# Performance work log

Hardware: AMD Instinct MI355X
Metric: run time of the kernel (lower is better)

Reference implementation:

```python
import jax, jax.numpy as jnp
import numpy as np

B, C, H, W = 4, 256, 64, 64
EPS = 1e-6


def setup_inputs() -> dict:
    key = jax.random.key(0)
    ks = jax.random.split(key, 6)
    x = jax.random.normal(ks[0], (B, C, H, W), jnp.float32)
    gn_w = jnp.ones((1, C, 1, 1), jnp.float32)
    gn_b = jnp.zeros((1, C, 1, 1), jnp.float32)
    s = 1.0 / np.sqrt(C)
    w0 = jax.random.normal(ks[1], (C, C), jnp.float32) * s
    w1 = jax.random.normal(ks[2], (C, C), jnp.float32) * s
    w2 = jax.random.normal(ks[3], (C, C), jnp.float32) * s
    w3 = jax.random.normal(ks[4], (C, C), jnp.float32) * s
    b0 = jnp.zeros((C,), jnp.float32)
    b1 = jnp.zeros((C,), jnp.float32)
    b2 = jnp.zeros((C,), jnp.float32)
    b3 = jnp.zeros((C,), jnp.float32)
    return {"x": x, "gn_w": gn_w, "gn_b": gn_b,
            "w0": w0, "b0": b0, "w1": w1, "b1": b1,
            "w2": w2, "b2": b2, "w3": w3, "b3": b3}


def _nin(t, Wm, bv):
    # 1x1 conv as channel matmul: (B,C,H,W) x (C,D) -> (B,D,H,W)
    return jnp.einsum('bchw,cd->bdhw', t, Wm) + bv[None, :, None, None]


def reference(x, gn_w, gn_b, w0, b0, w1, b1, w2, b2, w3, b3):
    Bb, Cc, Hh, Ww = x.shape
    G = min(Cc // 4, 32)  # GroupLayerNorm2d groups
    # per-pixel group norm: normalize over channels within each group only
    xg = x.reshape(Bb, G, Cc // G, Hh, Ww)
    mean = xg.mean(axis=2, keepdims=True)
    var = xg.var(axis=2, keepdims=True)
    hn = ((xg - mean) / jnp.sqrt(var + EPS)).reshape(Bb, Cc, Hh, Ww)
    hn = hn * gn_w + gn_b
    q = _nin(hn, w0, b0)
    k = _nin(hn, w1, b1)
    v = _nin(hn, w2, b2)
    # full (B,H,W,H,W) scores; mask is causal along W only (key col j > query col w)
    scores = jnp.einsum('bchw,bcij->bhwij', q, k) * (float(Cc) ** -0.5)
    causal = jnp.triu(jnp.ones((Ww, Ww), bool), k=1)  # (W_query, W_key)
    scores = jnp.where(causal[None, None, :, None, :], -jnp.inf, scores)
    attn = jax.nn.softmax(scores.reshape(Bb, Hh, Ww, Hh * Ww), axis=-1)
    attn = attn.reshape(Bb, Hh, Ww, Hh, Ww)
    h = jnp.einsum('bhwij,bcij->bchw', attn, v)
    return x + _nin(h, w3, b3)  # skip_rescale=False
```

## Files before the change

### kernel.cpp

```cpp
#include <hip/hip_runtime.h>
#include <math.h>

#define LOG2E 1.4426950408889634f

typedef __attribute__((ext_vector_type(8))) __bf16 bf16x8_t;
typedef __attribute__((ext_vector_type(8))) short short8_t;
typedef __attribute__((ext_vector_type(4))) short short4_t;
typedef __attribute__((ext_vector_type(4))) float f32x4;

static __device__ __forceinline__ short f2bf(float f){
    unsigned u = __builtin_bit_cast(unsigned, f);
    unsigned r = (u + 0x7fffu + ((u >> 16) & 1u)) >> 16;
    return (short)r;
}
static __device__ __forceinline__ float bf2f(short s){
    return __builtin_bit_cast(float, (unsigned)((unsigned short)s) << 16);
}

static __device__ __forceinline__ f32x4 mfma16(short8_t a, short8_t b, f32x4 c){
    return __builtin_amdgcn_mfma_f32_16x16x32_bf16(
        __builtin_bit_cast(bf16x8_t, a), __builtin_bit_cast(bf16x8_t, b), c, 0, 0, 0);
}

static __device__ __forceinline__ float swz16(float v){
    return __builtin_bit_cast(float,
        __builtin_amdgcn_ds_swizzle(__builtin_bit_cast(int, v), 0x401F));
}
static __device__ __forceinline__ float bperm32(int addr, float v){
    return __builtin_bit_cast(float,
        __builtin_amdgcn_ds_bpermute(addr, __builtin_bit_cast(int, v)));
}

__global__ __launch_bounds__(256) void prep_w(const float* __restrict__ w0,
    const float* __restrict__ w1, const float* __restrict__ w2,
    const float* __restrict__ w3, short* __restrict__ wT)
{
    __shared__ float T[64 * 65];
    const int mat = blockIdx.x >> 4, tile = blockIdx.x & 15;
    const int c0 = (tile >> 2) * 64, d0 = (tile & 3) * 64;
    const float* src = mat == 0 ? w0 : mat == 1 ? w1 : mat == 2 ? w2 : w3;
    const int t = threadIdx.x;
    #pragma unroll
    for (int i = 0; i < 4; i++){
        int r = (t >> 4) + i * 16, c4 = (t & 15) * 4;
        f32x4 v = *(const f32x4*)(src + (size_t)(c0 + r) * 256 + d0 + c4);
        #pragma unroll
        for (int j = 0; j < 4; j++) T[r * 65 + c4 + j] = v[j];
    }
    __syncthreads();
    int drow = t >> 2, cb = (t & 3) * 16;
    short tmp[16];
    #pragma unroll
    for (int j = 0; j < 16; j++) tmp[j] = f2bf(T[(cb + j) * 65 + drow]);
    short* dst = wT + (size_t)mat * 65536 + (size_t)(d0 + drow) * 256 + c0 + cb;
    *(short8_t*)dst = *(short8_t*)tmp;
    *(short8_t*)(dst + 8) = *(short8_t*)(tmp + 8);
}

__global__ __launch_bounds__(256) void gn_kernel(const float* __restrict__ x,
    const float* __restrict__ gnw, const float* __restrict__ gnb,
    short* __restrict__ hn)
{
    int flat = blockIdx.x * 256 + threadIdx.x;
    int n = flat & 4095, g = (flat >> 12) & 31, b = flat >> 17;
    const float* xp = x + (size_t)(b * 256 + g * 8) * 4096 + n;
    float v[8], s = 0.f, s2 = 0.f;
    #pragma unroll
    for (int k = 0; k < 8; k++){ float t = xp[(size_t)k * 4096]; v[k] = t; s += t; s2 += t * t; }
    float mean = s * 0.125f;
    float var  = s2 * 0.125f - mean * mean;
    float inv  = rsqrtf(var + 1e-6f);
    int h = n >> 6, w = n & 63, m = w * 64 + h;
    short o[8];
    #pragma unroll
    for (int k = 0; k < 8; k++)
        o[k] = f2bf((v[k] - mean) * inv * gnw[g * 8 + k] + gnb[g * 8 + k]);
    *(short8_t*)(hn + (size_t)(b * 4096 + m) * 256 + g * 8) = *(short8_t*)o;
}

__global__ __launch_bounds__(256) void qkv_gemm(const short* __restrict__ hn,
    const short* __restrict__ wT, const float* __restrict__ bq,
    const float* __restrict__ bk, const float* __restrict__ bv,
    short* __restrict__ Q, short* __restrict__ Kf, short* __restrict__ Vf)
{
    __shared__ short As[64 * 72];
    __shared__ short Bs[64 * 72];
    __shared__ float CT[64 * 65];

    const int tid = threadIdx.x;
    const int m0 = blockIdx.x * 64;
    const int by = blockIdx.y;
    const int mat = by >> 2;
    const int d0 = (by & 3) * 64;
    const short* w = wT + mat * 65536;
    const float* bias = mat == 0 ? bq : mat == 1 ? bk : bv;

    const int wv = tid >> 6, lane = tid & 63;
    const int wrow = (wv >> 1) * 32, wcol = (wv & 1) * 32;
    const int lrow = lane & 15, lq = lane >> 4;

    f32x4 acc[2][2] = {};

    for (int k0 = 0; k0 < 256; k0 += 64){
        __syncthreads();
        #pragma unroll
        for (int i = 0; i < 2; i++){
            int idx = tid + i * 256, r = idx >> 3, c = (idx & 7) * 8;
            *(short8_t*)&As[r * 72 + c] = *(const short8_t*)(hn + (size_t)(m0 + r) * 256 + k0 + c);
            *(short8_t*)&Bs[r * 72 + c] = *(const short8_t*)(w  + (size_t)(d0 + r) * 256 + k0 + c);
        }
        __syncthreads();
        #pragma unroll
        for (int kk = 0; kk < 2; kk++){
            int off = kk * 32 + lq * 8;
            short8_t a0  = *(short8_t*)&As[(wrow + lrow) * 72 + off];
            short8_t a1  = *(short8_t*)&As[(wrow + 16 + lrow) * 72 + off];
            short8_t b0v = *(short8_t*)&Bs[(wcol + lrow) * 72 + off];
            short8_t b1v = *(short8_t*)&Bs[(wcol + 16 + lrow) * 72 + off];
            acc[0][0] = mfma16(a0, b0v, acc[0][0]);
            acc[0][1] = mfma16(a0, b1v, acc[0][1]);
            acc[1][0] = mfma16(a1, b0v, acc[1][0]);
            acc[1][1] = mfma16(a1, b1v, acc[1][1]);
        }
    }

    const int b = m0 >> 12, kb64 = (m0 & 4095) >> 6;

    if (mat == 0){
        #pragma unroll
        for (int i = 0; i < 2; i++)
          #pragma unroll
          for (int j = 0; j < 2; j++)
            #pragma unroll
            for (int r = 0; r < 4; r++){
                int row = wrow + i * 16 + lq * 4 + r;
                int col = wcol + j * 16 + lrow;
                Q[(size_t)(m0 + row) * 256 + d0 + col] = f2bf((acc[i][j][r] + bias[d0 + col]) * 0.0625f);
            }
    } else if (mat == 1){
        #pragma unroll
        for (int i = 0; i < 2; i++)
          #pragma unroll
          for (int j = 0; j < 2; j++)
            #pragma unroll
            for (int r = 0; r < 4; r++){
                int row = wrow + i * 16 + lq * 4 + r;
                int col = wcol + j * 16 + lrow;
                CT[row * 65 + col] = acc[i][j][r] + bias[d0 + col];
            }
        __syncthreads();
        int key = tid >> 2, c16 = (tid & 3) * 16;
        int kc = key >> 4, l15 = key & 15;
        #pragma unroll
        for (int half = 0; half < 2; half++){
            int ch0 = c16 + half * 8;
            int ks = (d0 + ch0) >> 5, lqf = (ch0 & 31) >> 3;
            short tmp[8];
            #pragma unroll
            for (int j = 0; j < 8; j++) tmp[j] = f2bf(CT[key * 65 + ch0 + j]);
            size_t base = ((((size_t)(b * 64 + kb64)) * 4 + kc) * 8 + ks) * 512 + (lqf * 16 + l15) * 8;
            *(short8_t*)(Kf + base) = *(short8_t*)tmp;
        }
    } else {
        #pragma unroll
        for (int i = 0; i < 2; i++)
          #pragma unroll
          for (int j = 0; j < 2; j++)
            #pragma unroll
            for (int r = 0; r < 4; r++){
                int row = wrow + i * 16 + lq * 4 + r;
                int col = wcol + j * 16 + lrow;
                CT[col * 65 + row] = acc[i][j][r] + bias[d0 + col];
            }
        __syncthreads();
        const int kbd = kb64 >> 1, parity = kb64 & 1;
        const int cht_l = tid >> 6, lane_s = tid & 63;
        const int l15s = lane_s & 15, lg4s = lane_s >> 4;
        const int cht = (d0 >> 4) + cht_l;
        #pragma unroll
        for (int kc = 0; kc < 4; kc++){
            short tmp[4];
            #pragma unroll
            for (int j = 0; j < 4; j++)
                tmp[j] = f2bf(CT[(cht_l * 16 + l15s) * 65 + kc * 16 + lg4s * 4 + j]);
            size_t base = (size_t)b * 1048576 + (size_t)kbd * 32768 + kc * 8192
                        + cht * 512 + lane_s * 8 + parity * 4;
            *(short4_t*)(Vf + base) = *(short4_t*)tmp;
        }
    }
}

__global__ __launch_bounds__(256, 2) void attn_kernel(const short* __restrict__ Q,
    const short* __restrict__ Kf, const short* __restrict__ Vf,
    short* __restrict__ hb)
{
    __shared__ float mls[4][16][2];
    __shared__ short LOs[4][16][264];

    const int tid = threadIdx.x, lane = tid & 63, kc = tid >> 6;
    const int l15 = lane & 15, lg4 = lane >> 4;
    const int a32 = ((lane ^ 32) << 2);

    const int id = blockIdx.x;
    const int qd = id >> 8, c = id & 255;
    const int w6 = c >> 2, hh = (c >> 1) & 1, rg = c & 1;
    const int b  = qd;
    const int w  = (qd & 1) ? 63 - w6 : w6;
    const int q0 = w * 64 + hh * 32 + rg * 16;

    const short* Kb = Kf + (size_t)b * 1048576 + kc * 4096 + lane * 8;
    const short* Vb = Vf + (size_t)b * 1048576 + kc * 8192 + lane * 8;

    short8_t qf[8];
    {
        const short* qp = Q + ((size_t)b * 4096 + q0 + l15) * 256;
        #pragma unroll
        for (int ks = 0; ks < 8; ks++)
            qf[ks] = *(const short8_t*)(qp + ks * 32 + lg4 * 8);
    }

    f32x4 oacc[16] = {};
    float m_run = -1e30f, l_run = 0.f;

    short8_t kcur[8], knext[8];
    #pragma unroll
    for (int ks = 0; ks < 8; ks++)
        kcur[ks] = *(const short8_t*)(Kb + ks * 512);

    for (int kb = 0; kb <= w; kb += 2){
        const bool has_odd = (kb + 1 <= w);
        if (has_odd){
            const short* kit = Kb + (size_t)(kb + 1) * 16384;
            #pragma unroll
            for (int ks = 0; ks < 8; ks++)
                knext[ks] = *(const short8_t*)(kit + ks * 512);
        }
        f32x4 st = {};
        #pragma unroll
        for (int ks = 0; ks < 8; ks++) st = mfma16(kcur[ks], qf[ks], st);

        if (kb + 2 <= w){
            const short* kit = Kb + (size_t)(kb + 2) * 16384;
            #pragma unroll
            for (int ks = 0; ks < 8; ks++)
                kcur[ks] = *(const short8_t*)(kit + ks * 512);
        }

        f32x4 st2 = { -1e30f, -1e30f, -1e30f, -1e30f };
        if (has_odd){
            f32x4 z = {};
            #pragma unroll
            for (int ks = 0; ks < 8; ks++) z = mfma16(knext[ks], qf[ks], z);
            st2 = z;
        }

        float tmax = fmaxf(fmaxf(fmaxf(st[0], st[1]), fmaxf(st[2], st[3])),
                           fmaxf(fmaxf(st2[0], st2[1]), fmaxf(st2[2], st2[3])));
        tmax = fmaxf(tmax, swz16(tmax));
        tmax = fmaxf(tmax, bperm32(a32, tmax));
        float m_new = fmaxf(m_run, tmax);
        float alpha = exp2f((m_run - m_new) * LOG2E);
        m_run = m_new;

        f32x4 p_e, p_o;
        #pragma unroll
        for (int r = 0; r < 4; r++){
            p_e[r] = exp2f((st[r]  - m_new) * LOG2E);
            p_o[r] = exp2f((st2[r] - m_new) * LOG2E);
        }
        float tsum = ((p_e[0] + p_e[1]) + (p_e[2] + p_e[3]))
                   + ((p_o[0] + p_o[1]) + (p_o[2] + p_o[3]));
        tsum += swz16(tsum);
        tsum += bperm32(a32, tsum);
        l_run = l_run * alpha + tsum;

        short pb[8];
        #pragma unroll
        for (int r = 0; r < 4; r++){ pb[r] = f2bf(p_e[r]); pb[4 + r] = f2bf(p_o[r]); }
        short8_t pbf = *(short8_t*)pb;

        const short* vit = Vb + (size_t)(kb >> 1) * 32768;
        #pragma unroll
        for (int cht = 0; cht < 16; cht++){
            short8_t vfr = *(const short8_t*)(vit + cht * 512);
            f32x4 t = oacc[cht];
            #pragma unroll
            for (int r = 0; r < 4; r++) t[r] *= alpha;
            oacc[cht] = mfma16(vfr, pbf, t);
        }
    }

    if (lg4 == 0){ mls[kc][l15][0] = m_run; mls[kc][l15][1] = l_run; }
    __syncthreads();
    float m0v = mls[0][l15][0], m1v = mls[1][l15][0], m2v = mls[2][l15][0], m3v = mls[3][l15][0];
    float mstar = fmaxf(fmaxf(m0v, m1v), fmaxf(m2v, m3v));
    float Lsum = mls[0][l15][1] * exp2f((m0v - mstar) * LOG2E)
               + mls[1][l15][1] * exp2f((m1v - mstar) * LOG2E)
               + mls[2][l15][1] * exp2f((m2v - mstar) * LOG2E)
               + mls[3][l15][1] * exp2f((m3v - mstar) * LOG2E);
    float sc = exp2f((m_run - mstar) * LOG2E);
    #pragma unroll
    for (int cht = 0; cht < 16; cht++){
        short t4[4];
        #pragma unroll
        for (int r = 0; r < 4; r++) t4[r] = f2bf(oacc[cht][r] * sc);
        *(short4_t*)&LOs[kc][l15][cht * 16 + lg4 * 4] = *(short4_t*)t4;
    }
    __syncthreads();
    {
        const int ch0 = kc * 64 + lg4 * 16;
        float inv = 1.f / Lsum;
        short tmp[16];
        #pragma unroll
        for (int c8 = 0; c8 < 2; c8++){
            short8_t a0 = *(const short8_t*)&LOs[0][l15][ch0 + c8 * 8];
            short8_t a1 = *(const short8_t*)&LOs[1][l15][ch0 + c8 * 8];
            short8_t a2 = *(const short8_t*)&LOs[2][l15][ch0 + c8 * 8];
            short8_t a3 = *(const short8_t*)&LOs[3][l15][ch0 + c8 * 8];
            #pragma unroll
            for (int j = 0; j < 8; j++){
                float s = (bf2f(a0[j]) + bf2f(a1[j])) + (bf2f(a2[j]) + bf2f(a3[j]));
                tmp[c8 * 8 + j] = f2bf(s * inv);
            }
        }
        const int h = hh * 32 + rg * 16 + l15;
        short* dst = hb + ((size_t)b * 4096 + h * 64 + w) * 256 + ch0;
        *(short8_t*)dst = *(short8_t*)tmp;
        *(short8_t*)(dst + 8) = *(short8_t*)(tmp + 8);
    }
}

__global__ __launch_bounds__(256) void final_gemm(const short* __restrict__ hbuf,
    const short* __restrict__ wT3, const float* __restrict__ b3,
    const float* __restrict__ x, float* __restrict__ out)
{
    __shared__ short As[64 * 72];
    __shared__ short Bs[64 * 72];
    __shared__ float CT[64 * 65];

    const int tid = threadIdx.x;
    const int m0 = blockIdx.x * 64;
    const int d0 = blockIdx.y * 64;
    const int wv = tid >> 6, lane = tid & 63;
    const int wrow = (wv >> 1) * 32, wcol = (wv & 1) * 32;
    const int lrow = lane & 15, lq = lane >> 4;

    f32x4 acc[2][2] = {};
    for (int k0 = 0; k0 < 256; k0 += 64){
        __syncthreads();
        #pragma unroll
        for (int i = 0; i < 2; i++){
            int idx = tid + i * 256, r = idx >> 3, c = (idx & 7) * 8;
            *(short8_t*)&As[r * 72 + c] = *(const short8_t*)(hbuf + (size_t)(m0 + r) * 256 + k0 + c);
            *(short8_t*)&Bs[r * 72 + c] = *(const short8_t*)(wT3 + (size_t)(d0 + r) * 256 + k0 + c);
        }
        __syncthreads();
        #pragma unroll
        for (int kk = 0; kk < 2; kk++){
            int off = kk * 32 + lq * 8;
            short8_t a0  = *(short8_t*)&As[(wrow + lrow) * 72 + off];
            short8_t a1  = *(short8_t*)&As[(wrow + 16 + lrow) * 72 + off];
            short8_t b0v = *(short8_t*)&Bs[(wcol + lrow) * 72 + off];
            short8_t b1v = *(short8_t*)&Bs[(wcol + 16 + lrow) * 72 + off];
            acc[0][0] = mfma16(a0, b0v, acc[0][0]);
            acc[0][1] = mfma16(a0, b1v, acc[0][1]);
            acc[1][0] = mfma16(a1, b0v, acc[1][0]);
            acc[1][1] = mfma16(a1, b1v, acc[1][1]);
        }
    }
    #pragma unroll
    for (int i = 0; i < 2; i++)
      #pragma unroll
      for (int j = 0; j < 2; j++)
        #pragma unroll
        for (int r = 0; r < 4; r++){
            int row = wrow + i * 16 + lq * 4 + r;
            int col = wcol + j * 16 + lrow;
            CT[col * 65 + row] = acc[i][j][r] + b3[d0 + col];
        }
    __syncthreads();
    int b = m0 >> 12, n0 = m0 & 4095, hrow = n0 >> 6;
    int dr = tid >> 2, wc = (tid & 3) * 16;
    size_t base = ((size_t)(b * 256 + d0 + dr) * 64 + hrow) * 64 + wc;
    const f32x4* xp = (const f32x4*)(x + base);
    f32x4* op = (f32x4*)(out + base);
    #pragma unroll
    for (int q = 0; q < 4; q++){
        f32x4 xv = xp[q], o;
        #pragma unroll
        for (int j = 0; j < 4; j++) o[j] = xv[j] + CT[dr * 65 + wc + q * 4 + j];
        op[q] = o;
    }
}

extern "C" void kernel_launch(void* const* d_in, const int* in_sizes, int n_in,
                              void* d_out, int out_size, void* d_ws, size_t ws_size,
                              hipStream_t stream)
{
    const float* x   = (const float*)d_in[0];
    const float* gnw = (const float*)d_in[1];
    const float* gnb = (const float*)d_in[2];
    const float* w0  = (const float*)d_in[3];
    const float* b0  = (const float*)d_in[4];
    const float* w1  = (const float*)d_in[5];
    const float* b1  = (const float*)d_in[6];
    const float* w2  = (const float*)d_in[7];
    const float* b2  = (const float*)d_in[8];
    const float* w3  = (const float*)d_in[9];
    const float* b3  = (const float*)d_in[10];
    float* out = (float*)d_out;

    char* ws = (char*)d_ws;
    short* wT  = (short*)(ws);
    short* hn  = (short*)(ws + 524288);
    short* Qb  = (short*)(ws + 8912896);
    short* Kfb = (short*)(ws + 17301504);
    short* Vfb = (short*)(ws + 25690112);
    short* hb  = (short*)(ws + 34078720);

    prep_w   <<<64, 256, 0, stream>>>(w0, w1, w2, w3, wT);
    gn_kernel<<<2048, 256, 0, stream>>>(x, gnw, gnb, hn);
    qkv_gemm <<<dim3(256, 12), 256, 0, stream>>>(hn, wT, b0, b1, b2, Qb, Kfb, Vfb);
    attn_kernel<<<1024, 256, 0, stream>>>(Qb, Kfb, Vfb, hb);
    final_gemm<<<dim3(256, 4), 256, 0, stream>>>(hb, wT + 3 * 65536, b3, x, out);
}
```

Before: 210.6 us.

## Process two query tiles per block to reuse K/V loads, add lazy softmax rescaling

Each attention block now handles 32 query rows (two 16-row MFMA tiles) instead of 16, so every K and V fragment loaded from memory feeds two MFMAs, halving global K/V traffic per query. The grid shrinks to 512 blocks and is remapped so batch and row-half are keyed on block index modulo 8, which appears aimed at XCD-local cache reuse. The online softmax skips the accumulator rescale unless the max grows by more than a threshold, which saves VALU multiplies but depends on the exp values staying bounded. The cost is doubled accumulator registers, which may cut occupancy, and half as many blocks.

After: 244.3 us. 1.16x slower.

```diff
diff --git a/kernel.cpp b/kernel.cpp
--- a/kernel.cpp
+++ b/kernel.cpp
@@ -190,143 +190,175 @@
     }
 }
 
+static __device__ __forceinline__ void sm_update(const f32x4& st, float& m, float& l,
+    f32x4* __restrict__ oacc, f32x4* __restrict__ pa, f32x4& p, int a32)
+{
+    float tmax = fmaxf(fmaxf(st[0], st[1]), fmaxf(st[2], st[3]));
+    tmax = fmaxf(tmax, swz16(tmax));
+    tmax = fmaxf(tmax, bperm32(a32, tmax));
+    if (!__all(tmax <= m + 5.0f)){
+        float mn = fmaxf(m, tmax);
+        float alpha = exp2f((m - mn) * LOG2E);
+        l *= alpha;
+        #pragma unroll
+        for (int i = 0; i < 16; i++){
+            f32x4 t = oacc[i];
+            #pragma unroll
+            for (int r = 0; r < 4; r++) t[r] *= alpha;
+            oacc[i] = t;
+        }
+        if (pa){
+            #pragma unroll
+            for (int r = 0; r < 4; r++) (*pa)[r] *= alpha;
+        }
+        m = mn;
+    }
+    #pragma unroll
+    for (int r = 0; r < 4; r++) p[r] = exp2f((st[r] - m) * LOG2E);
+    float ts = (p[0] + p[1]) + (p[2] + p[3]);
+    ts += swz16(ts);
+    ts += bperm32(a32, ts);
+    l += ts;
+}
+
 __global__ __launch_bounds__(256, 2) void attn_kernel(const short* __restrict__ Q,
     const short* __restrict__ Kf, const short* __restrict__ Vf,
     short* __restrict__ hb)
 {
-    __shared__ float mls[4][16][2];
-    __shared__ short LOs[4][16][264];
+    __shared__ float mls[4][32][2];
+    __shared__ short LOs[4][32][264];
 
     const int tid = threadIdx.x, lane = tid & 63, kc = tid >> 6;
     const int l15 = lane & 15, lg4 = lane >> 4;
     const int a32 = ((lane ^ 32) << 2);
 
-    const int id = blockIdx.x;
-    const int qd = id >> 8, c = id & 255;
-    const int w6 = c >> 2, hh = (c >> 1) & 1, rg = c & 1;
-    const int b  = qd;
-    const int w  = (qd & 1) ? 63 - w6 : w6;
-    const int q0 = w * 64 + hh * 32 + rg * 16;
+    const int id  = blockIdx.x;
+    const int xcd = id & 7;
+    const int b   = xcd >> 1;
+    const int hh  = xcd & 1;
+    const int r_  = id >> 3;
+    const int t_  = r_ & 31;
+    const int w   = (r_ >> 5) ? 63 - t_ : t_;
+    const int q0  = w * 64 + hh * 32;
 
     const short* Kb = Kf + (size_t)b * 1048576 + kc * 4096 + lane * 8;
     const short* Vb = Vf + (size_t)b * 1048576 + kc * 8192 + lane * 8;
 
-    short8_t qf[8];
+    short8_t qf0[8], qf1[8];
     {
-        const short* qp = Q + ((size_t)b * 4096 + q0 + l15) * 256;
-        #pragma unroll
-        for (int ks = 0; ks < 8; ks++)
-            qf[ks] = *(const short8_t*)(qp + ks * 32 + lg4 * 8);
-    }
-
-    f32x4 oacc[16] = {};
-    float m_run = -1e30f, l_run = 0.f;
-
-    short8_t kcur[8], knext[8];
-    #pragma unroll
-    for (int ks = 0; ks < 8; ks++)
-        kcur[ks] = *(const short8_t*)(Kb + ks * 512);
+        const short* qp0 = Q + ((size_t)b * 4096 + q0 + l15) * 256;
+        const short* qp1 = qp0 + 16 * 256;
+        #pragma unroll
+        for (int ks = 0; ks < 8; ks++){
+            qf0[ks] = *(const short8_t*)(qp0 + ks * 32 + lg4 * 8);
+            qf1[ks] = *(const short8_t*)(qp1 + ks * 32 + lg4 * 8);
+        }
+    }
+
+    f32x4 oacc0[16] = {}, oacc1[16] = {};
+    float m0 = -1e30f, l0 = 0.f;
+    float m1 = -1e30f, l1 = 0.f;
 
     for (int kb = 0; kb <= w; kb += 2){
-        const bool has_odd = (kb + 1 <= w);
-        if (has_odd){
-            const short* kit = Kb + (size_t)(kb + 1) * 16384;
-            #pragma unroll
-            for (int ks = 0; ks < 8; ks++)
-                knext[ks] = *(const short8_t*)(kit + ks * 512);
-        }
-        f32x4 st = {};
-        #pragma unroll
-        for (int ks = 0; ks < 8; ks++) st = mfma16(kcur[ks], qf[ks], st);
-
-        if (kb + 2 <= w){
-            const short* kit = Kb + (size_t)(kb + 2) * 16384;
-            #pragma unroll
-            for (int ks = 0; ks < 8; ks++)
-                kcur[ks] = *(const short8_t*)(kit + ks * 512);
-        }
-
-        f32x4 st2 = { -1e30f, -1e30f, -1e30f, -1e30f };
-        if (has_odd){
-            f32x4 z = {};
-            #pragma unroll
-            for (int ks = 0; ks < 8; ks++) z = mfma16(knext[ks], qf[ks], z);
-            st2 = z;
-        }
-
-        float tmax = fmaxf(fmaxf(fmaxf(st[0], st[1]), fmaxf(st[2], st[3])),
-                           fmaxf(fmaxf(st2[0], st2[1]), fmaxf(st2[2], st2[3])));
-        tmax = fmaxf(tmax, swz16(tmax));
-        tmax = fmaxf(tmax, bperm32(a32, tmax));
-        float m_new = fmaxf(m_run, tmax);
-        float alpha = exp2f((m_run - m_new) * LOG2E);
-        m_run = m_new;
-
-        f32x4 p_e, p_o;
+        short8_t kf[8];
+        {
+            const short* ka = Kb + (size_t)kb * 16384;
+            #pragma unroll
+            for (int ks = 0; ks < 8; ks++) kf[ks] = *(const short8_t*)(ka + ks * 512);
+        }
+        f32x4 stA0 = {}, stA1 = {};
+        #pragma unroll
+        for (int ks = 0; ks < 8; ks++){
+            stA0 = mfma16(kf[ks], qf0[ks], stA0);
+            stA1 = mfma16(kf[ks], qf1[ks], stA1);
+        }
+        f32x4 pa0, pa1;
+        sm_update(stA0, m0, l0, oacc0, nullptr, pa0, a32);
+        sm_update(stA1, m1, l1, oacc1, nullptr, pa1, a32);
+
+        f32x4 pb0 = {0.f, 0.f, 0.f, 0.f}, pb1 = {0.f, 0.f, 0.f, 0.f};
+        if (kb + 1 <= w){
+            const short* ka = Kb + (size_t)(kb + 1) * 16384;
+            #pragma unroll
+            for (int ks = 0; ks < 8; ks++) kf[ks] = *(const short8_t*)(ka + ks * 512);
+            f32x4 stB0 = {}, stB1 = {};
+            #pragma unroll
+            for (int ks = 0; ks < 8; ks++){
+                stB0 = mfma16(kf[ks], qf0[ks], stB0);
+                stB1 = mfma16(kf[ks], qf1[ks], stB1);
+            }
+            sm_update(stB0, m0, l0, oacc0, &pa0, pb0, a32);
+            sm_update(stB1, m1, l1, oacc1, &pa1, pb1, a32);
+        }
+
+        short pk0[8], pk1[8];
         #pragma unroll
         for (int r = 0; r < 4; r++){
-            p_e[r] = exp2f((st[r]  - m_new) * LOG2E);
-            p_o[r] = exp2f((st2[r] - m_new) * LOG2E);
-        }
-        float tsum = ((p_e[0] + p_e[1]) + (p_e[2] + p_e[3]))
-                   + ((p_o[0] + p_o[1]) + (p_o[2] + p_o[3]));
-        tsum += swz16(tsum);
-        tsum += bperm32(a32, tsum);
-        l_run = l_run * alpha + tsum;
-
-        short pb[8];
-        #pragma unroll
-        for (int r = 0; r < 4; r++){ pb[r] = f2bf(p_e[r]); pb[4 + r] = f2bf(p_o[r]); }
-        short8_t pbf = *(short8_t*)pb;
+            pk0[r] = f2bf(pa0[r]); pk0[4 + r] = f2bf(pb0[r]);
+            pk1[r] = f2bf(pa1[r]); pk1[4 + r] = f2bf(pb1[r]);
+        }
+        short8_t pbf0 = *(short8_t*)pk0;
+        short8_t pbf1 = *(short8_t*)pk1;
 
         const short* vit = Vb + (size_t)(kb >> 1) * 32768;
         #pragma unroll
         for (int cht = 0; cht < 16; cht++){
             short8_t vfr = *(const short8_t*)(vit + cht * 512);
-            f32x4 t = oacc[cht];
-            #pragma unroll
-            for (int r = 0; r < 4; r++) t[r] *= alpha;
-            oacc[cht] = mfma16(vfr, pbf, t);
-        }
-    }
-
-    if (lg4 == 0){ mls[kc][l15][0] = m_run; mls[kc][l15][1] = l_run; }
+            oacc0[cht] = mfma16(vfr, pbf0, oacc0[cht]);
+            oacc1[cht] = mfma16(vfr, pbf1, oacc1[cht]);
+        }
+    }
+
+    if (lg4 == 0){
+        mls[kc][l15][0] = m0;      mls[kc][l15][1] = l0;
+        mls[kc][16 + l15][0] = m1; mls[kc][16 + l15][1] = l1;
+    }
     __syncthreads();
-    float m0v = mls[0][l15][0], m1v = mls[1][l15][0], m2v = mls[2][l15][0], m3v = mls[3][l15][0];
-    float mstar = fmaxf(fmaxf(m0v, m1v), fmaxf(m2v, m3v));
-    float Lsum = mls[0][l15][1] * exp2f((m0v - mstar) * LOG2E)
-               + mls[1][l15][1] * exp2f((m1v - mstar) * LOG2E)
-               + mls[2][l15][1] * exp2f((m2v - mstar) * LOG2E)
-               + mls[3][l15][1] * exp2f((m3v - mstar) * LOG2E);
-    float sc = exp2f((m_run - mstar) * LOG2E);
+    float sc0, sc1;
+    {
+        float ms0 = fmaxf(fmaxf(mls[0][l15][0], mls[1][l15][0]),
+                          fmaxf(mls[2][l15][0], mls[3][l15][0]));
+        float ms1 = fmaxf(fmaxf(mls[0][16 + l15][0], mls[1][16 + l15][0]),
+                          fmaxf(mls[2][16 + l15][0], mls[3][16 + l15][0]));
+        sc0 = exp2f((m0 - ms0) * LOG2E);
+        sc1 = exp2f((m1 - ms1) * LOG2E);
+    }
     #pragma unroll
     for (int cht = 0; cht < 16; cht++){
         short t4[4];
         #pragma unroll
-        for (int r = 0; r < 4; r++) t4[r] = f2bf(oacc[cht][r] * sc);
+        for (int r = 0; r < 4; r++) t4[r] = f2bf(oacc0[cht][r] * sc0);
         *(short4_t*)&LOs[kc][l15][cht * 16 + lg4 * 4] = *(short4_t*)t4;
+        #pragma unroll
+        for (int r = 0; r < 4; r++) t4[r] = f2bf(oacc1[cht][r] * sc1);
+        *(short4_t*)&LOs[kc][16 + l15][cht * 16 + lg4 * 4] = *(short4_t*)t4;
     }
     __syncthreads();
     {
-        const int ch0 = kc * 64 + lg4 * 16;
-        float inv = 1.f / Lsum;
-        short tmp[16];
-        #pragma unroll
-        for (int c8 = 0; c8 < 2; c8++){
-            short8_t a0 = *(const short8_t*)&LOs[0][l15][ch0 + c8 * 8];
-            short8_t a1 = *(const short8_t*)&LOs[1][l15][ch0 + c8 * 8];
-            short8_t a2 = *(const short8_t*)&LOs[2][l15][ch0 + c8 * 8];
-            short8_t a3 = *(const short8_t*)&LOs[3][l15][ch0 + c8 * 8];
+        const int qq = tid & 31, cc = tid >> 5;
+        float mv0 = mls[0][qq][0], mv1 = mls[1][qq][0], mv2 = mls[2][qq][0], mv3 = mls[3][qq][0];
+        float ms = fmaxf(fmaxf(mv0, mv1), fmaxf(mv2, mv3));
+        float Ls = mls[0][qq][1] * exp2f((mv0 - ms) * LOG2E)
+                 + mls[1][qq][1] * exp2f((mv1 - ms) * LOG2E)
+                 + mls[2][qq][1] * exp2f((mv2 - ms) * LOG2E)
+                 + mls[3][qq][1] * exp2f((mv3 - ms) * LOG2E);
+        float inv = 1.f / Ls;
+        const int h = hh * 32 + qq;
+        short* dst = hb + ((size_t)b * 4096 + h * 64 + w) * 256 + cc * 32;
+        #pragma unroll
+        for (int c8 = 0; c8 < 4; c8++){
+            short8_t a0 = *(const short8_t*)&LOs[0][qq][cc * 32 + c8 * 8];
+            short8_t a1 = *(const short8_t*)&LOs[1][qq][cc * 32 + c8 * 8];
+            short8_t a2 = *(const short8_t*)&LOs[2][qq][cc * 32 + c8 * 8];
+            short8_t a3 = *(const short8_t*)&LOs[3][qq][cc * 32 + c8 * 8];
+            short t8[8];
             #pragma unroll
             for (int j = 0; j < 8; j++){
                 float s = (bf2f(a0[j]) + bf2f(a1[j])) + (bf2f(a2[j]) + bf2f(a3[j]));
-                tmp[c8 * 8 + j] = f2bf(s * inv);
+                t8[j] = f2bf(s * inv);
             }
-        }
-        const int h = hh * 32 + rg * 16 + l15;
-        short* dst = hb + ((size_t)b * 4096 + h * 64 + w) * 256 + ch0;
-        *(short8_t*)dst = *(short8_t*)tmp;
-        *(short8_t*)(dst + 8) = *(short8_t*)(tmp + 8);
+            *(short8_t*)(dst + c8 * 8) = *(short8_t*)t8;
+        }
     }
 }
 
@@ -421,6 +453,6 @@
     prep_w   <<<64, 256, 0, stream>>>(w0, w1, w2, w3, wT);
     gn_kernel<<<2048, 256, 0, stream>>>(x, gnw, gnb, hn);
     qkv_gemm <<<dim3(256, 12), 256, 0, stream>>>(hn, wT, b0, b1, b2, Qb, Kfb, Vfb);
-    attn_kernel<<<1024, 256, 0, stream>>>(Qb, Kfb, Vfb, hb);
+    attn_kernel<<<512, 256, 0, stream>>>(Qb, Kfb, Vfb, hb);
     final_gemm<<<dim3(256, 4), 256, 0, stream>>>(hb, wT + 3 * 65536, b3, x, out);
 }
```
